# Performance work log

Hardware: AMD Instinct MI355X
Metric: run time of the kernel (lower is better)

The kernel has to match this reference:

```python
import jax, jax.numpy as jnp
import numpy as np

B = 131072      # batch of states
N_ACT = 40      # output_dim (Tetris action space)


def setup_inputs() -> dict:
    key = jax.random.key(0)
    ks = jax.random.split(key, 9)
    # state vector: 11 real-valued board features, 1 hold-piece id in [0,4),
    # 3 next-piece ids in [1,8) (0 is treated as invalid by the original code)
    keep = jax.random.normal(ks[0], (B, 11), dtype=jnp.float32)
    hold = jax.random.randint(ks[1], (B, 1), 0, 4).astype(jnp.float32)
    nxt = jax.random.randint(ks[2], (B, 3), 1, 8).astype(jnp.float32)
    x = jnp.concatenate([keep, hold, nxt], axis=1)  # [B, 15]
    W1 = jax.random.normal(ks[3], (36, 128), dtype=jnp.float32) * 0.1
    b1 = jnp.zeros((128,), dtype=jnp.float32)
    W2 = jax.random.normal(ks[4], (128, 512), dtype=jnp.float32) * 0.05
    b2 = jnp.zeros((512,), dtype=jnp.float32)
    W4 = jax.random.normal(ks[5], (512, N_ACT), dtype=jnp.float32) * 0.05
    b4 = jnp.zeros((N_ACT,), dtype=jnp.float32)
    return {"x": x, "W1": W1, "b1": b1, "W2": W2, "b2": b2, "W4": W4, "b4": b4}


def reference(x, W1, b1, W2, b2, W4, b4):
    B_, _ = x.shape
    keep = x[:, :11]                                      # [B, 11]
    # vectorized replacement of the per-sample .item() one-hot loop
    hold_idx = jax.lax.stop_gradient(jnp.clip(x[:, 11].astype(jnp.int32), 0, 3))
    nxt_idx = jax.lax.stop_gradient(jnp.clip(x[:, 12:15].astype(jnp.int32) - 1, 0, 6))
    hold_oh = jax.nn.one_hot(hold_idx, 4, dtype=x.dtype)  # [B, 4]
    nxt_oh = jax.nn.one_hot(nxt_idx, 7, dtype=x.dtype).reshape(B_, 21)  # [B, 21]
    inp = jnp.concatenate([keep, hold_oh, nxt_oh], axis=1)  # [B, 36]
    h = jax.nn.relu(inp @ W1 + b1)   # [B, 128]
    h = jax.nn.relu(h @ W2 + b2)     # [B, 512]
    return h @ W4 + b4               # [B, N_ACT]
```

## Files before the change

### kernel.cpp

```cpp
#include <hip/hip_runtime.h>


typedef short bf16x8 __attribute__((ext_vector_type(8)));
typedef float f32x4 __attribute__((ext_vector_type(4)));
typedef unsigned int u32;

#define NW1F 8192
#define NW2F 65536
#define NW4F 24576
#define PACK_TOTAL (NW1F + NW2F + NW4F)
#define PACK_THREADS (PACK_TOTAL / 8)

#define SROW 136

__device__ __forceinline__ unsigned short f2bf(float f) {
  union { float f; unsigned u; } a; a.f = f;
  unsigned r = a.u + 0x7fffu + ((a.u >> 16) & 1u);
  return (unsigned short)(r >> 16);
}
__device__ __forceinline__ u32 cvtpk(float lo, float hi) {
  u32 r;
  asm("v_cvt_pk_bf16_f32 %0, %1, %2" : "=v"(r) : "v"(lo), "v"(hi));
  return r;
}

__global__ void pack_weights(const float* __restrict__ W1,
                             const float* __restrict__ W2,
                             const float* __restrict__ W4,
                             unsigned short* __restrict__ wf) {
  int t = blockIdx.x * 256 + threadIdx.x;
  if (t >= PACK_THREADS) return;
  int fid = t >> 6, lane = t & 63;
  int l16 = lane & 15, quad = lane >> 4;
  float vals[8];
  if (fid < 16) {
    int mt = fid >> 1, ks = fid & 1;
    int m = mt * 16 + l16, k0 = ks * 32 + quad * 8;
#pragma unroll
    for (int j = 0; j < 8; ++j) { int k = k0 + j; vals[j] = (k < 36) ? W1[k * 128 + m] : 0.f; }
  } else if (fid < 144) {
    int f = fid - 16, mt = f >> 2, ks = f & 3;
    int m = mt * 16 + l16, k0 = ks * 32 + quad * 8;
#pragma unroll
    for (int j = 0; j < 8; ++j) vals[j] = W2[(k0 + j) * 512 + m];
  } else {
    int f = fid - 144, mt = f >> 4, ks = f & 15;
    int m = mt * 16 + l16, k0 = ks * 32 + quad * 8;
#pragma unroll
    for (int j = 0; j < 8; ++j) vals[j] = (m < 40) ? W4[(k0 + j) * 40 + m] : 0.f;
  }
  u32 p[4];
#pragma unroll
  for (int j = 0; j < 4; ++j) p[j] = cvtpk(vals[2 * j], vals[2 * j + 1]);
  *(bf16x8*)(wf + (size_t)t * 8) = *(bf16x8*)p;
}

#define MTL_STEP(chunk, mtl, hb)                                               \
  {                                                                            \
    int fb = (chunk) * 16 + (mtl) * 4 + 4;                                     \
    if (fb >= 128) fb = 0;           \
    _Pragma("unroll")                                                          \
    for (int k = 0; k < 4; ++k)                                                \
      W[((mtl) + 1) & 1][k] = *(const bf16x8*)(w2p + (size_t)(fb + k) * 512);  \
    f32x4 acc2[4];                                                             \
    _Pragma("unroll")                                                          \
    for (int rg = 0; rg < 4; ++rg) acc2[rg] = bias2[mtl];                      \
    __builtin_amdgcn_s_setprio(1);                                             \
    _Pragma("unroll")                                                          \
    for (int ks = 0; ks < 4; ++ks)                                             \
      _Pragma("unroll")                                                        \
      for (int rg = 0; rg < 4; ++rg)                                           \
        acc2[rg] = __builtin_amdgcn_mfma_f32_16x16x32_bf16(                    \
            W[(mtl) & 1][ks], af1[rg][ks], acc2[rg], 0, 0, 0);                 \
    __builtin_amdgcn_s_setprio(0);                                             \
    _Pragma("unroll")                                                          \
    for (int rg = 0; rg < 4; ++rg) {                                           \
      float v0 = fmaxf(acc2[rg][0], 0.f);                                      \
      float v1 = fmaxf(acc2[rg][1], 0.f);                                      \
      float v2 = fmaxf(acc2[rg][2], 0.f);                                      \
      float v3 = fmaxf(acc2[rg][3], 0.f);                                      \
      uint2 pk = {cvtpk(v0, v1), cvtpk(v2, v3)};                               \
      *(uint2*)(su + (rg * 16 + l16) * SROW + (hb) + (mtl) * 16 + quad * 4) = pk; \
    }                                                                          \
  }

#define H_READ(dst, hbp, ks3)                                                  \
  _Pragma("unroll")                                                            \
  for (int rg = 0; rg < 4; ++rg)                                               \
    dst[rg] = *(const bf16x8*)(su + (rg * 16 + l16) * SROW + (hbp) + (ks3) * 32 + quad * 8);

#define W4_LOAD(dst, chunkprev, ks3)                                           \
  _Pragma("unroll")                                                            \
  for (int mt3 = 0; mt3 < 3; ++mt3)                                            \
    dst[mt3] = *(const bf16x8*)(                                               \
        w4f + (size_t)((mt3 * 16 + (chunkprev) * 2 + (ks3)) * 64 + lane) * 8);

#define L3_PART(w4q, hq)                                                       \
  __builtin_amdgcn_s_setprio(1);                                               \
  _Pragma("unroll")                                                            \
  for (int mt3 = 0; mt3 < 3; ++mt3)                                            \
    _Pragma("unroll")                                                          \
    for (int rg = 0; rg < 4; ++rg)                                             \
      accO[mt3][rg] = __builtin_amdgcn_mfma_f32_16x16x32_bf16(                 \
          w4q[mt3], hq[rg], accO[mt3][rg], 0, 0, 0);                           \
  __builtin_amdgcn_s_setprio(0);

__global__ __launch_bounds__(128, 2) void dqn_fused(
    const float* __restrict__ x,
    const unsigned short* __restrict__ wf,
    const float* __restrict__ b1,
    const float* __restrict__ b2,
    const float* __restrict__ b4,
    float* __restrict__ out) {
  __shared__ __align__(16) unsigned short sBuf[2 * 64 * SROW];

  const int tid  = threadIdx.x;
  const int lane = tid & 63;
  const int wave = tid >> 6;
  const int quad = lane >> 4;
  const int l16  = lane & 15;
  const int row0 = blockIdx.x << 7;
  const int lr0  = wave * 64;
  unsigned short* su = sBuf + wave * (64 * SROW);

  const unsigned short* w2f = wf + NW1F;
  const unsigned short* w4f = wf + NW1F + NW2F;
  const unsigned short* w2p = w2f + lane * 8;

  bf16x8 W[2][4];
#pragma unroll
  for (int k = 0; k < 4; ++k) W[0][k] = *(const bf16x8*)(w2p + (size_t)k * 512);

  {
    const float* xr = x + (size_t)(row0 + lr0 + lane) * 15;
    unsigned short* dst = su + lane * SROW;
    bf16x8 z = {0, 0, 0, 0, 0, 0, 0, 0};
#pragma unroll
    for (int c = 8; c < 64; c += 8) *(bf16x8*)(dst + c) = z;
    u32 p[4];
#pragma unroll
    for (int i = 0; i < 4; ++i) p[i] = cvtpk(xr[2 * i], xr[2 * i + 1]);
    *(bf16x8*)dst = *(bf16x8*)p;
    *(u32*)(dst + 8) = cvtpk(xr[8], xr[9]);
    dst[10] = f2bf(xr[10]);
    int hold = (int)xr[11]; hold = hold < 0 ? 0 : (hold > 3 ? 3 : hold);
    dst[11 + hold] = 0x3F80;
#pragma unroll
    for (int t = 0; t < 3; ++t) {
      int nx = (int)xr[12 + t] - 1; nx = nx < 0 ? 0 : (nx > 6 ? 6 : nx);
      dst[15 + t * 7 + nx] = 0x3F80;
    }
  }

  const f32x4 vzero = {0.f, 0.f, 0.f, 0.f};

  bf16x8 ib[4][2];
#pragma unroll
  for (int rg = 0; rg < 4; ++rg)
#pragma unroll
    for (int ks = 0; ks < 2; ++ks)
      ib[rg][ks] = *(const bf16x8*)(su + (rg * 16 + l16) * SROW + ks * 32 + quad * 8);

  bf16x8 af1[4][4];
#pragma unroll
  for (int half = 0; half < 2; ++half) {
    bf16x8 wa[4][2];
#pragma unroll
    for (int mtl = 0; mtl < 4; ++mtl)
#pragma unroll
      for (int ks = 0; ks < 2; ++ks)
        wa[mtl][ks] = *(const bf16x8*)(
            wf + (size_t)(((half * 4 + mtl) * 2 + ks) * 64 + lane) * 8);

    f32x4 acc1[4][4];
#pragma unroll
    for (int mtl = 0; mtl < 4; ++mtl) {
      f32x4 bias = *(const f32x4*)(b1 + (half * 4 + mtl) * 16 + quad * 4);
#pragma unroll
      for (int rg = 0; rg < 4; ++rg) acc1[mtl][rg] = bias;
    }

    __builtin_amdgcn_s_setprio(1);
#pragma unroll
    for (int mtl = 0; mtl < 4; ++mtl)
#pragma unroll
      for (int ks = 0; ks < 2; ++ks)
#pragma unroll
        for (int rg = 0; rg < 4; ++rg)
          acc1[mtl][rg] = __builtin_amdgcn_mfma_f32_16x16x32_bf16(wa[mtl][ks], ib[rg][ks], acc1[mtl][rg], 0, 0, 0);
    __builtin_amdgcn_s_setprio(0);

#pragma unroll
    for (int mtl = 0; mtl < 4; ++mtl) {
#pragma unroll
      for (int rg = 0; rg < 4; ++rg) {
        float v0 = fmaxf(acc1[mtl][rg][0], 0.f);
        float v1 = fmaxf(acc1[mtl][rg][1], 0.f);
        float v2 = fmaxf(acc1[mtl][rg][2], 0.f);
        float v3 = fmaxf(acc1[mtl][rg][3], 0.f);
        uint2 pk = {cvtpk(v0, v1), cvtpk(v2, v3)};
        *(uint2*)(su + (rg * 16 + l16) * SROW + mtl * 16 + quad * 4) = pk;
      }
    }
#pragma unroll
    for (int rg = 0; rg < 4; ++rg)
#pragma unroll
      for (int ksl = 0; ksl < 2; ++ksl)
        af1[rg][half * 2 + ksl] =
            *(const bf16x8*)(su + (rg * 16 + l16) * SROW + ksl * 32 + quad * 8);
  }

  f32x4 accO[3][4];
#pragma unroll
  for (int mt = 0; mt < 3; ++mt)
#pragma unroll
    for (int rg = 0; rg < 4; ++rg) accO[mt][rg] = vzero;

  {
    f32x4 bias2[4];
#pragma unroll
    for (int mtl = 0; mtl < 4; ++mtl)
      bias2[mtl] = *(const f32x4*)(b2 + mtl * 16 + quad * 4);
    MTL_STEP(0, 0, 0)
    MTL_STEP(0, 1, 0)
    MTL_STEP(0, 2, 0)
    MTL_STEP(0, 3, 0)
  }
  for (int chunk = 1; chunk < 8; ++chunk) {
    const int hb  = (chunk & 1) * 72;
    const int hbp = 72 - hb;
    f32x4 bias2[4];
#pragma unroll
    for (int mtl = 0; mtl < 4; ++mtl)
      bias2[mtl] = *(const f32x4*)(b2 + chunk * 64 + mtl * 16 + quad * 4);

    bf16x8 w4a[3];
    W4_LOAD(w4a, chunk - 1, 0)
    MTL_STEP(chunk, 0, hb)
    bf16x8 h0[4];
    H_READ(h0, hbp, 0)
    MTL_STEP(chunk, 1, hb)
    L3_PART(w4a, h0)
    bf16x8 w4b[3];
    W4_LOAD(w4b, chunk - 1, 1)
    MTL_STEP(chunk, 2, hb)
    bf16x8 h1v[4];
    H_READ(h1v, hbp, 1)
    MTL_STEP(chunk, 3, hb)
    L3_PART(w4b, h1v)
  }
  {
    bf16x8 w4a[3];
    W4_LOAD(w4a, 7, 0)
    bf16x8 h0[4];
    H_READ(h0, 72, 0)
    L3_PART(w4a, h0)
    bf16x8 w4b[3];
    W4_LOAD(w4b, 7, 1)
    bf16x8 h1v[4];
    H_READ(h1v, 72, 1)
    L3_PART(w4b, h1v)
  }

#pragma unroll
  for (int mt3 = 0; mt3 < 3; ++mt3) {
    int colbase = mt3 * 16 + quad * 4;
    if (colbase < 40) {
      f32x4 bias = *(const f32x4*)(b4 + colbase);
#pragma unroll
      for (int rg = 0; rg < 4; ++rg) {
        f32x4 v = accO[mt3][rg] + bias;
        size_t row = (size_t)(row0 + lr0 + rg * 16 + l16);
        *(f32x4*)(out + row * 40 + colbase) = v;
      }
    }
  }
}

extern "C" void kernel_launch(void* const* d_in, const int* in_sizes, int n_in,
                              void* d_out, int out_size, void* d_ws, size_t ws_size,
                              hipStream_t stream) {
  const float* x  = (const float*)d_in[0];
  const float* W1 = (const float*)d_in[1];
  const float* b1 = (const float*)d_in[2];
  const float* W2 = (const float*)d_in[3];
  const float* b2 = (const float*)d_in[4];
  const float* W4 = (const float*)d_in[5];
  const float* b4 = (const float*)d_in[6];
  float* out = (float*)d_out;
  unsigned short* wf = (unsigned short*)d_ws;

  int B = in_sizes[0] / 15;

  hipLaunchKernelGGL(pack_weights, dim3((PACK_THREADS + 255) / 256), dim3(256), 0, stream,
                     W1, W2, W4, wf);
  hipLaunchKernelGGL(dqn_fused, dim3(B / 128), dim3(128), 0, stream,
                     x, wf, b1, b2, b4, out);
}
```

Before: 96.62 us.

## Halve rows per wave to 32, single-buffer hidden chunk, raise occupancy to 4 blocks

Each wave now handles 32 rows instead of 64, which halves the accumulator and activation register arrays. Launch bounds go to 4 blocks per CU and the grid is doubled. The layer-2 hidden chunk in LDS is single-buffered instead of double-buffered: the previous chunk is read into registers before being overwritten, and the bias is folded into the first MFMA. The cost is that every W2 and W4 fragment loaded per wave is reused over half as many rows, so weight load traffic per row doubles, traded for more waves in flight to hide latency.

```diff
diff --git a/kernel.cpp b/kernel.cpp
--- a/kernel.cpp
+++ b/kernel.cpp
@@ -11,7 +11,7 @@
 #define PACK_TOTAL (NW1F + NW2F + NW4F)
 #define PACK_THREADS (PACK_TOTAL / 8)
 
-#define SROW 136
+#define SROW 72
 
 __device__ __forceinline__ unsigned short f2bf(float f) {
   union { float f; unsigned u; } a; a.f = f;
@@ -55,39 +55,42 @@
   *(bf16x8*)(wf + (size_t)t * 8) = *(bf16x8*)p;
 }
 
-#define MTL_STEP(chunk, mtl, hb)                                               \
+#define MTL_STEP(chunk, mtl)                                                   \
   {                                                                            \
+    f32x4 bias2 = *(const f32x4*)(b2 + (chunk) * 64 + (mtl) * 16 + quad * 4);  \
     int fb = (chunk) * 16 + (mtl) * 4 + 4;                                     \
     if (fb >= 128) fb = 0;           \
     _Pragma("unroll")                                                          \
     for (int k = 0; k < 4; ++k)                                                \
       W[((mtl) + 1) & 1][k] = *(const bf16x8*)(w2p + (size_t)(fb + k) * 512);  \
-    f32x4 acc2[4];                                                             \
-    _Pragma("unroll")                                                          \
-    for (int rg = 0; rg < 4; ++rg) acc2[rg] = bias2[mtl];                      \
+    f32x4 acc2[2];                                                             \
     __builtin_amdgcn_s_setprio(1);                                             \
     _Pragma("unroll")                                                          \
-    for (int ks = 0; ks < 4; ++ks)                                             \
+    for (int rg = 0; rg < 2; ++rg)                                             \
+      acc2[rg] = __builtin_amdgcn_mfma_f32_16x16x32_bf16(                      \
+          W[(mtl) & 1][0], af1[rg][0], bias2, 0, 0, 0);                        \
+    _Pragma("unroll")                                                          \
+    for (int ks = 1; ks < 4; ++ks)                                             \
       _Pragma("unroll")                                                        \
-      for (int rg = 0; rg < 4; ++rg)                                           \
+      for (int rg = 0; rg < 2; ++rg)                                           \
         acc2[rg] = __builtin_amdgcn_mfma_f32_16x16x32_bf16(                    \
             W[(mtl) & 1][ks], af1[rg][ks], acc2[rg], 0, 0, 0);                 \
     __builtin_amdgcn_s_setprio(0);                                             \
     _Pragma("unroll")                                                          \
-    for (int rg = 0; rg < 4; ++rg) {                                           \
+    for (int rg = 0; rg < 2; ++rg) {                                           \
       float v0 = fmaxf(acc2[rg][0], 0.f);                                      \
       float v1 = fmaxf(acc2[rg][1], 0.f);                                      \
       float v2 = fmaxf(acc2[rg][2], 0.f);                                      \
       float v3 = fmaxf(acc2[rg][3], 0.f);                                      \
       uint2 pk = {cvtpk(v0, v1), cvtpk(v2, v3)};                               \
-      *(uint2*)(su + (rg * 16 + l16) * SROW + (hb) + (mtl) * 16 + quad * 4) = pk; \
+      *(uint2*)(su + (rg * 16 + l16) * SROW + (mtl) * 16 + quad * 4) = pk;     \
     }                                                                          \
   }
 
-#define H_READ(dst, hbp, ks3)                                                  \
+#define H_READ(dst, ks3)                                                       \
   _Pragma("unroll")                                                            \
-  for (int rg = 0; rg < 4; ++rg)                                               \
-    dst[rg] = *(const bf16x8*)(su + (rg * 16 + l16) * SROW + (hbp) + (ks3) * 32 + quad * 8);
+  for (int rg = 0; rg < 2; ++rg)                                               \
+    dst[rg] = *(const bf16x8*)(su + (rg * 16 + l16) * SROW + (ks3) * 32 + quad * 8);
 
 #define W4_LOAD(dst, chunkprev, ks3)                                           \
   _Pragma("unroll")                                                            \
@@ -100,28 +103,28 @@
   _Pragma("unroll")                                                            \
   for (int mt3 = 0; mt3 < 3; ++mt3)                                            \
     _Pragma("unroll")                                                          \
-    for (int rg = 0; rg < 4; ++rg)                                             \
+    for (int rg = 0; rg < 2; ++rg)                                             \
       accO[mt3][rg] = __builtin_amdgcn_mfma_f32_16x16x32_bf16(                 \
           w4q[mt3], hq[rg], accO[mt3][rg], 0, 0, 0);                           \
   __builtin_amdgcn_s_setprio(0);
 
-__global__ __launch_bounds__(128, 2) void dqn_fused(
+__global__ __launch_bounds__(128, 4) void dqn_fused(
     const float* __restrict__ x,
     const unsigned short* __restrict__ wf,
     const float* __restrict__ b1,
     const float* __restrict__ b2,
     const float* __restrict__ b4,
     float* __restrict__ out) {
-  __shared__ __align__(16) unsigned short sBuf[2 * 64 * SROW];
+  __shared__ __align__(16) unsigned short sBuf[2 * 32 * SROW];
 
   const int tid  = threadIdx.x;
   const int lane = tid & 63;
   const int wave = tid >> 6;
   const int quad = lane >> 4;
   const int l16  = lane & 15;
-  const int row0 = blockIdx.x << 7;
-  const int lr0  = wave * 64;
-  unsigned short* su = sBuf + wave * (64 * SROW);
+  const int row0 = blockIdx.x << 6;
+  const int lr0  = wave * 32;
+  unsigned short* su = sBuf + wave * (32 * SROW);
 
   const unsigned short* w2f = wf + NW1F;
   const unsigned short* w4f = wf + NW1F + NW2F;
@@ -131,7 +134,7 @@
 #pragma unroll
   for (int k = 0; k < 4; ++k) W[0][k] = *(const bf16x8*)(w2p + (size_t)k * 512);
 
-  {
+  if (lane < 32) {
     const float* xr = x + (size_t)(row0 + lr0 + lane) * 15;
     unsigned short* dst = su + lane * SROW;
     bf16x8 z = {0, 0, 0, 0, 0, 0, 0, 0};
@@ -154,14 +157,14 @@
 
   const f32x4 vzero = {0.f, 0.f, 0.f, 0.f};
 
-  bf16x8 ib[4][2];
-#pragma unroll
-  for (int rg = 0; rg < 4; ++rg)
+  bf16x8 ib[2][2];
+#pragma unroll
+  for (int rg = 0; rg < 2; ++rg)
 #pragma unroll
     for (int ks = 0; ks < 2; ++ks)
       ib[rg][ks] = *(const bf16x8*)(su + (rg * 16 + l16) * SROW + ks * 32 + quad * 8);
 
-  bf16x8 af1[4][4];
+  bf16x8 af1[2][4];
 #pragma unroll
   for (int half = 0; half < 2; ++half) {
     bf16x8 wa[4][2];
@@ -172,93 +175,72 @@
         wa[mtl][ks] = *(const bf16x8*)(
             wf + (size_t)(((half * 4 + mtl) * 2 + ks) * 64 + lane) * 8);
 
-    f32x4 acc1[4][4];
 #pragma unroll
     for (int mtl = 0; mtl < 4; ++mtl) {
-      f32x4 bias = *(const f32x4*)(b1 + (half * 4 + mtl) * 16 + quad * 4);
-#pragma unroll
-      for (int rg = 0; rg < 4; ++rg) acc1[mtl][rg] = bias;
-    }
-
-    __builtin_amdgcn_s_setprio(1);
-#pragma unroll
-    for (int mtl = 0; mtl < 4; ++mtl)
-#pragma unroll
-      for (int ks = 0; ks < 2; ++ks)
-#pragma unroll
-        for (int rg = 0; rg < 4; ++rg)
-          acc1[mtl][rg] = __builtin_amdgcn_mfma_f32_16x16x32_bf16(wa[mtl][ks], ib[rg][ks], acc1[mtl][rg], 0, 0, 0);
-    __builtin_amdgcn_s_setprio(0);
-
-#pragma unroll
-    for (int mtl = 0; mtl < 4; ++mtl) {
-#pragma unroll
-      for (int rg = 0; rg < 4; ++rg) {
-        float v0 = fmaxf(acc1[mtl][rg][0], 0.f);
-        float v1 = fmaxf(acc1[mtl][rg][1], 0.f);
-        float v2 = fmaxf(acc1[mtl][rg][2], 0.f);
-        float v3 = fmaxf(acc1[mtl][rg][3], 0.f);
+      f32x4 bias1 = *(const f32x4*)(b1 + (half * 4 + mtl) * 16 + quad * 4);
+      f32x4 acc1[2];
+      __builtin_amdgcn_s_setprio(1);
+#pragma unroll
+      for (int rg = 0; rg < 2; ++rg)
+        acc1[rg] = __builtin_amdgcn_mfma_f32_16x16x32_bf16(wa[mtl][0], ib[rg][0], bias1, 0, 0, 0);
+#pragma unroll
+      for (int rg = 0; rg < 2; ++rg)
+        acc1[rg] = __builtin_amdgcn_mfma_f32_16x16x32_bf16(wa[mtl][1], ib[rg][1], acc1[rg], 0, 0, 0);
+      __builtin_amdgcn_s_setprio(0);
+#pragma unroll
+      for (int rg = 0; rg < 2; ++rg) {
+        float v0 = fmaxf(acc1[rg][0], 0.f);
+        float v1 = fmaxf(acc1[rg][1], 0.f);
+        float v2 = fmaxf(acc1[rg][2], 0.f);
+        float v3 = fmaxf(acc1[rg][3], 0.f);
         uint2 pk = {cvtpk(v0, v1), cvtpk(v2, v3)};
         *(uint2*)(su + (rg * 16 + l16) * SROW + mtl * 16 + quad * 4) = pk;
       }
     }
 #pragma unroll
-    for (int rg = 0; rg < 4; ++rg)
+    for (int rg = 0; rg < 2; ++rg)
 #pragma unroll
       for (int ksl = 0; ksl < 2; ++ksl)
         af1[rg][half * 2 + ksl] =
             *(const bf16x8*)(su + (rg * 16 + l16) * SROW + ksl * 32 + quad * 8);
   }
 
-  f32x4 accO[3][4];
+  f32x4 accO[3][2];
 #pragma unroll
   for (int mt = 0; mt < 3; ++mt)
 #pragma unroll
-    for (int rg = 0; rg < 4; ++rg) accO[mt][rg] = vzero;
-
-  {
-    f32x4 bias2[4];
-#pragma unroll
-    for (int mtl = 0; mtl < 4; ++mtl)
-      bias2[mtl] = *(const f32x4*)(b2 + mtl * 16 + quad * 4);
-    MTL_STEP(0, 0, 0)
-    MTL_STEP(0, 1, 0)
-    MTL_STEP(0, 2, 0)
-    MTL_STEP(0, 3, 0)
-  }
+    for (int rg = 0; rg < 2; ++rg) accO[mt][rg] = vzero;
+
+  MTL_STEP(0, 0)
+  MTL_STEP(0, 1)
+  MTL_STEP(0, 2)
+  MTL_STEP(0, 3)
   for (int chunk = 1; chunk < 8; ++chunk) {
-    const int hb  = (chunk & 1) * 72;
-    const int hbp = 72 - hb;
-    f32x4 bias2[4];
-#pragma unroll
-    for (int mtl = 0; mtl < 4; ++mtl)
-      bias2[mtl] = *(const f32x4*)(b2 + chunk * 64 + mtl * 16 + quad * 4);
-
+    bf16x8 h0[2];
+    H_READ(h0, 0)
+    MTL_STEP(chunk, 0)
+    MTL_STEP(chunk, 1)
     bf16x8 w4a[3];
     W4_LOAD(w4a, chunk - 1, 0)
-    MTL_STEP(chunk, 0, hb)
-    bf16x8 h0[4];
-    H_READ(h0, hbp, 0)
-    MTL_STEP(chunk, 1, hb)
     L3_PART(w4a, h0)
+    bf16x8 h1v[2];
+    H_READ(h1v, 1)
+    MTL_STEP(chunk, 2)
+    MTL_STEP(chunk, 3)
     bf16x8 w4b[3];
     W4_LOAD(w4b, chunk - 1, 1)
-    MTL_STEP(chunk, 2, hb)
-    bf16x8 h1v[4];
-    H_READ(h1v, hbp, 1)
-    MTL_STEP(chunk, 3, hb)
     L3_PART(w4b, h1v)
   }
   {
+    bf16x8 h0[2];
+    H_READ(h0, 0)
+    bf16x8 h1v[2];
+    H_READ(h1v, 1)
     bf16x8 w4a[3];
     W4_LOAD(w4a, 7, 0)
-    bf16x8 h0[4];
-    H_READ(h0, 72, 0)
     L3_PART(w4a, h0)
     bf16x8 w4b[3];
     W4_LOAD(w4b, 7, 1)
-    bf16x8 h1v[4];
-    H_READ(h1v, 72, 1)
     L3_PART(w4b, h1v)
   }
 
@@ -268,7 +250,7 @@
     if (colbase < 40) {
       f32x4 bias = *(const f32x4*)(b4 + colbase);
 #pragma unroll
-      for (int rg = 0; rg < 4; ++rg) {
+      for (int rg = 0; rg < 2; ++rg) {
         f32x4 v = accO[mt3][rg] + bias;
         size_t row = (size_t)(row0 + lr0 + rg * 16 + l16);
         *(f32x4*)(out + row * 40 + colbase) = v;
@@ -294,6 +276,6 @@
 
   hipLaunchKernelGGL(pack_weights, dim3((PACK_THREADS + 255) / 256), dim3(256), 0, stream,
                      W1, W2, W4, wf);
-  hipLaunchKernelGGL(dqn_fused, dim3(B / 128), dim3(128), 0, stream,
+  hipLaunchKernelGGL(dqn_fused, dim3(B / 64), dim3(128), 0, stream,
                      x, wf, b1, b2, b4, out);
 }
```

Measured after the change: 111.4 us. +15.3%, slower.
